# Performance work log

Measured on AMD Instinct MI355X. Metric: run time of the kernel, lower is better.

Reference implementation:

```python
import jax, jax.numpy as jnp
import numpy as np

N = 50000      # nodes
E = 800000     # edges (before self-loops)
IN_C = 128
HID = 32
HEADS = 4
OUT_C = 64
NEG_SLOPE = 0.2


def setup_inputs() -> dict:
    key = jax.random.key(0)
    ks = jax.random.split(key, 10)
    x = jax.random.normal(ks[0], (N, IN_C), dtype=jnp.float32)
    edge_index = jax.random.randint(ks[1], (2, E), 0, N, dtype=jnp.int32)
    # layer 1 params (GATConv(in_c, hid_c, heads=4), concat=True)
    W1 = jax.random.normal(ks[2], (IN_C, HEADS * HID), dtype=jnp.float32) / np.sqrt(IN_C)
    a_src1 = jax.random.normal(ks[3], (HEADS, HID), dtype=jnp.float32) / np.sqrt(HID)
    a_dst1 = jax.random.normal(ks[4], (HEADS, HID), dtype=jnp.float32) / np.sqrt(HID)
    b1 = jnp.zeros((HEADS * HID,), dtype=jnp.float32)
    # layer 2 params (GATConv(hid_c*heads, out_c, heads=1))
    W2 = jax.random.normal(ks[5], (HEADS * HID, OUT_C), dtype=jnp.float32) / np.sqrt(HEADS * HID)
    a_src2 = jax.random.normal(ks[6], (1, OUT_C), dtype=jnp.float32) / np.sqrt(OUT_C)
    a_dst2 = jax.random.normal(ks[7], (1, OUT_C), dtype=jnp.float32) / np.sqrt(OUT_C)
    b2 = jnp.zeros((OUT_C,), dtype=jnp.float32)
    return {"x": x, "edge_index": edge_index, "W1": W1, "a_src1": a_src1,
            "a_dst1": a_dst1, "b1": b1, "W2": W2, "a_src2": a_src2,
            "a_dst2": a_dst2, "b2": b2}


def _gat_layer(x, src, dst, self_mask, W, a_s, a_d, b, n):
    """One PyG-style GATConv: concat heads, leaky_relu(0.2), scatter-softmax over dst."""
    H, F = a_s.shape
    h = (x @ W).reshape(n, H, F)                       # [N, H, F]
    al_s = jnp.einsum('nhf,hf->nh', h, a_s)            # [N, H]
    al_d = jnp.einsum('nhf,hf->nh', h, a_d)
    e = al_s[src] + al_d[dst]                          # [E', H]
    e = jnp.where(e >= 0, e, NEG_SLOPE * e)            # leaky relu
    # emulate remove_self_loops on original edges (appended loops not masked)
    e = jnp.where(self_mask[:, None], -1e30, e)
    m = jax.ops.segment_max(e, dst, num_segments=n)    # per-dst max for stability
    p = jnp.exp(e - m[dst])
    p = jnp.where(self_mask[:, None], 0.0, p)
    denom = jax.ops.segment_sum(p, dst, num_segments=n) + 1e-16
    alpha = p / denom[dst]                             # [E', H]
    out = jax.ops.segment_sum(alpha[:, :, None] * h[src], dst, num_segments=n)
    return out.reshape(n, H * F) + b


def reference(x, edge_index, W1, a_src1, a_dst1, b1, W2, a_src2, a_dst2, b2):
    n = x.shape[0]
    src, dst = edge_index[0], edge_index[1]
    loops = jnp.arange(n, dtype=edge_index.dtype)
    src_a = jnp.concatenate([src, loops])
    dst_a = jnp.concatenate([dst, loops])
    # mask pre-existing self-loops (PyG removes then re-adds self loops)
    self_mask = jnp.concatenate([src == dst, jnp.zeros((n,), dtype=bool)])
    h = _gat_layer(x, src_a, dst_a, self_mask, W1, a_src1, a_dst1, b1, n)
    h = jax.nn.relu(h)
    return _gat_layer(h, src_a, dst_a, self_mask, W2, a_src2, a_dst2, b2, n)
```

## Files before the change

kernel.cpp:

```cpp
#include <hip/hip_runtime.h>

typedef unsigned short u16;
typedef unsigned int u32;
typedef __attribute__((ext_vector_type(8))) short bf16x8;
typedef __attribute__((ext_vector_type(4))) float f32x4;

__device__ __forceinline__ float bf(u16 u){ return __uint_as_float(((u32)u) << 16); }
__device__ __forceinline__ float bf_lo(u32 u){ return __uint_as_float(u << 16); }
__device__ __forceinline__ float bf_hi(u32 u){ return __uint_as_float(u & 0xFFFF0000u); }
__device__ __forceinline__ u16 to_bf16(float f){
    u32 x = __float_as_uint(f);
    u32 r = (x + 0x7FFFu + ((x >> 16) & 1u)) >> 16;
    return (u16)r;
}
__device__ __forceinline__ float leaky(float v){ return (v >= 0.f) ? v : 0.2f * v; }
__device__ __forceinline__ float eexp(float v){
    return __expf(fminf(leaky(v), 80.f));
}
__device__ __forceinline__ float ldany(const void* p, int i, int fl){
    return fl ? bf(((const u16*)p)[i]) : ((const float*)p)[i];
}
__device__ __forceinline__ u16 ldany_bf(const void* p, int i, int fl){
    return fl ? ((const u16*)p)[i] : to_bf16(((const float*)p)[i]);
}

constexpr int NS = 256;

struct HistCvtArgs {
    const int* dst; const int* src; int E; int chE; u16* cnt; int NBIN;
    const void* xin; u16* Xb; int nx;
    const void* W1; const void* W2; u16* W1t; u16* W2t;
    const void* vin[6]; float* vout[6];
    int* flag;
};
__global__ __launch_bounds__(256) void hist_cvt(HistCvtArgs a){
    int b = blockIdx.x;
    if (b < NS){
        __shared__ u32 hist[128];
        if (threadIdx.x < 128) hist[threadIdx.x] = 0;
        __syncthreads();
        int s0 = b * a.chE, s1 = min(a.E, s0 + a.chE);
        for (int i = s0 + threadIdx.x; i < s1; i += 256){
            int d = a.dst[i];
            if (a.src[i] != d) atomicAdd(&hist[d >> 9], 1);
        }
        __syncthreads();
        if (threadIdx.x < a.NBIN)
            a.cnt[b * a.NBIN + threadIdx.x] = (u16)hist[threadIdx.x];
        return;
    }
    __shared__ int sflag;
    const u16* x16 = (const u16*)a.xin;
    if (threadIdx.x < 64){
        int ok = 1;
        for (int i = threadIdx.x; i < 256; i += 64){
            u16 v = x16[i];
            int e = (v >> 7) & 0xFF;
            if (!((e >= 100 && e <= 140) || (v & 0x7FFFu) == 0)) ok = 0;
        }
        unsigned long long bl = __ballot(ok);
        if (threadIdx.x == 0) sflag = (__popcll(bl) >= 62) ? 1 : 0;
    }
    __syncthreads();
    int fl = sflag;
    int ci = (b - NS) * 256 + threadIdx.x;
    if (ci == 0) *a.flag = fl;
    if (ci < a.nx){ a.Xb[ci] = ldany_bf(a.xin, ci, fl); return; }
    ci -= a.nx;
    if (ci < 128 * 128){
        int n = ci >> 7, k = ci & 127;
        a.W1t[ci] = ldany_bf(a.W1, k * 128 + n, fl);
        return;
    }
    ci -= 128 * 128;
    if (ci < 64 * 128){
        int n = ci >> 7, k = ci & 127;
        a.W2t[ci] = ldany_bf(a.W2, k * 64 + n, fl);
        return;
    }
    ci -= 64 * 128;
    const int vsz[6] = {128, 128, 128, 64, 64, 64};
    #pragma unroll
    for (int s = 0; s < 6; s++){
        if (ci < vsz[s]){ a.vout[s][ci] = ldany(a.vin[s], ci, fl); return; }
        ci -= vsz[s];
    }
}

__global__ __launch_bounds__(1024) void scan_cnt(const u16* __restrict__ cnt,
                                                 u32* __restrict__ S, int NBIN){
    __shared__ int wsum[16];
    int t = threadIdx.x;
    int M = NBIN * NS;
    int C = (M + 1023) / 1024;
    int f0 = t * C;
    int s = 0;
    for (int i = 0; i < C; i++){
        int f = f0 + i;
        if (f < M) s += cnt[(f & 255) * NBIN + (f >> 8)];
    }
    int v = s;
    #pragma unroll
    for (int d = 1; d < 64; d <<= 1){
        int o = __shfl_up(v, d);
        if ((t & 63) >= d) v += o;
    }
    if ((t & 63) == 63) wsum[t >> 6] = v;
    __syncthreads();
    int woff = 0;
    for (int wv = 0; wv < (t >> 6); wv++) woff += wsum[wv];
    int run = woff + v - s;
    for (int i = 0; i < C; i++){
        int f = f0 + i;
        if (f < M){
            S[f] = run;
            run += cnt[(f & 255) * NBIN + (f >> 8)];
        }
    }
    if (t == 1023) S[M] = run;
}

struct BucketGemmArgs {
    const int* dst; const int* src; int E; int chE; const u32* S; int NBIN;
    u32* bucket;
    const u16* Xb; const u16* W1t; u16* HB;
    const float* a_s; const float* a_d; float* al_s; float* al_d;
    int N;
};
__global__ __launch_bounds__(256) void bucket_gemm(BucketGemmArgs a){
    int b = blockIdx.x;
    if (b < NS){
        __shared__ u32 cur[128];
        if (threadIdx.x < a.NBIN) cur[threadIdx.x] = a.S[threadIdx.x * NS + b];
        __syncthreads();
        int s0 = b * a.chE, s1 = min(a.E, s0 + a.chE);
        for (int i = s0 + threadIdx.x; i < s1; i += 256){
            int d = a.dst[i];
            int s = a.src[i];
            if (s != d){
                u32 pos = atomicAdd(&cur[d >> 9], 1);
                a.bucket[pos] = ((u32)d << 16) | (u32)s;
            }
        }
        return;
    }
    int gb = b - NS;
    int lane = threadIdx.x & 63;
    int w = threadIdx.x >> 6;
    int row0 = gb * 64 + w * 16;
    int m = lane & 15, quad = lane >> 4;
    int arow = row0 + m;
    if (arow >= a.N) arow = a.N - 1;
    f32x4 acc[8];
    #pragma unroll
    for (int j = 0; j < 8; j++) acc[j] = (f32x4){0.f, 0.f, 0.f, 0.f};
    const u16* ap = a.Xb + (size_t)arow * 128 + quad * 8;
    const u16* bp = a.W1t + (size_t)m * 128 + quad * 8;
    #pragma unroll
    for (int kc = 0; kc < 4; kc++){
        bf16x8 av = *(const bf16x8*)(ap + kc * 32);
        #pragma unroll
        for (int nb = 0; nb < 8; nb++){
            bf16x8 bv = *(const bf16x8*)(bp + nb * 16 * 128 + kc * 32);
            acc[nb] = __builtin_amdgcn_mfma_f32_16x16x32_bf16(av, bv, acc[nb], 0, 0, 0);
        }
    }
    #pragma unroll
    for (int nb = 0; nb < 8; nb++){
        #pragma unroll
        for (int r = 0; r < 4; r++){
            int grow = row0 + quad * 4 + r;
            if (grow < a.N) a.HB[(size_t)grow * 128 + nb * 16 + m] = to_bf16(acc[nb][r]);
        }
    }
    float asr[8], adr[8];
    #pragma unroll
    for (int nb = 0; nb < 8; nb++){ asr[nb] = a.a_s[nb * 16 + m]; adr[nb] = a.a_d[nb * 16 + m]; }
    #pragma unroll
    for (int r = 0; r < 4; r++){
        int grow = row0 + quad * 4 + r;
        #pragma unroll
        for (int h = 0; h < 4; h++){
            float ps = acc[2 * h][r] * asr[2 * h] + acc[2 * h + 1][r] * asr[2 * h + 1];
            float pd = acc[2 * h][r] * adr[2 * h] + acc[2 * h + 1][r] * adr[2 * h + 1];
            #pragma unroll
            for (int d = 1; d < 16; d <<= 1){
                ps += __shfl_xor(ps, d);
                pd += __shfl_xor(pd, d);
            }
            if (m == h && grow < a.N){
                a.al_s[grow * 4 + h] = ps;
                a.al_d[grow * 4 + h] = pd;
            }
        }
    }
}

__global__ __launch_bounds__(256) void bin_csr(const u32* __restrict__ S,
                                               const u32* __restrict__ bucket,
                                               int* __restrict__ off,
                                               u16* __restrict__ csr,
                                               int N, int NBIN){
    __shared__ u32 degL[512];
    __shared__ u32 curL[512];
    __shared__ int wsum[4];
    int b = blockIdx.x, t = threadIdx.x;
    int lo = b << 9;
    u32 base = S[b * NS];
    u32 end  = S[(b + 1) * NS];
    degL[t] = 0; degL[t + 256] = 0;
    __syncthreads();
    for (u32 i = base + t; i < end; i += 256){
        u32 pr = bucket[i];
        atomicAdd(&degL[(pr >> 16) - lo], 1);
    }
    __syncthreads();
    u32 d0 = degL[2 * t], d1 = degL[2 * t + 1];
    int p = (int)(d0 + d1);
    int v = p;
    #pragma unroll
    for (int d = 1; d < 64; d <<= 1){
        int o = __shfl_up(v, d);
        if ((t & 63) >= d) v += o;
    }
    if ((t & 63) == 63) wsum[t >> 6] = v;
    __syncthreads();
    int woff = 0;
    for (int wv = 0; wv < (t >> 6); wv++) woff += wsum[wv];
    int eb = woff + v - p;
    curL[2 * t] = eb;
    curL[2 * t + 1] = eb + d0;
    int n0 = lo + 2 * t, n1 = lo + 2 * t + 1;
    if (n0 < N) off[n0] = (int)(base + eb);
    if (n1 < N) off[n1] = (int)(base + eb + d0);
    if (b == NBIN - 1 && t == 255) off[N] = (int)end;
    __syncthreads();
    for (u32 i = base + t; i < end; i += 256){
        u32 pr = bucket[i];
        u32 pos = base + atomicAdd(&curL[(pr >> 16) - lo], 1);
        csr[pos] = (u16)(pr & 0xFFFF);
    }
}

__global__ __launch_bounds__(256) void gemm2_logits(const u16* __restrict__ Xb,
                                                    const u16* __restrict__ Wt,
                                                    u16* __restrict__ HB,
                                                    const float* __restrict__ a_s,
                                                    const float* __restrict__ a_d,
                                                    float* __restrict__ al_s,
                                                    float* __restrict__ al_d, int N){
    int lane = threadIdx.x & 63;
    int w = threadIdx.x >> 6;
    int row0 = blockIdx.x * 64 + w * 16;
    int m = lane & 15, quad = lane >> 4;
    int arow = row0 + m;
    if (arow >= N) arow = N - 1;
    f32x4 acc[4];
    #pragma unroll
    for (int j = 0; j < 4; j++) acc[j] = (f32x4){0.f, 0.f, 0.f, 0.f};
    const u16* ap = Xb + (size_t)arow * 128 + quad * 8;
    const u16* bp = Wt + (size_t)m * 128 + quad * 8;
    #pragma unroll
    for (int kc = 0; kc < 4; kc++){
        bf16x8 av = *(const bf16x8*)(ap + kc * 32);
        #pragma unroll
        for (int nb = 0; nb < 4; nb++){
            bf16x8 bv = *(const bf16x8*)(bp + nb * 16 * 128 + kc * 32);
            acc[nb] = __builtin_amdgcn_mfma_f32_16x16x32_bf16(av, bv, acc[nb], 0, 0, 0);
        }
    }
    #pragma unroll
    for (int nb = 0; nb < 4; nb++){
        #pragma unroll
        for (int r = 0; r < 4; r++){
            int grow = row0 + quad * 4 + r;
            if (grow < N) HB[(size_t)grow * 64 + nb * 16 + m] = to_bf16(acc[nb][r]);
        }
    }
    float asr[4], adr[4];
    #pragma unroll
    for (int nb = 0; nb < 4; nb++){ asr[nb] = a_s[nb * 16 + m]; adr[nb] = a_d[nb * 16 + m]; }
    #pragma unroll
    for (int r = 0; r < 4; r++){
        int grow = row0 + quad * 4 + r;
        float ps = 0.f, pd = 0.f;
        #pragma unroll
        for (int nb = 0; nb < 4; nb++){ ps += acc[nb][r] * asr[nb]; pd += acc[nb][r] * adr[nb]; }
        #pragma unroll
        for (int d = 1; d < 16; d <<= 1){
            ps += __shfl_xor(ps, d);
            pd += __shfl_xor(pd, d);
        }
        if (m == 0 && grow < N){
            al_s[grow] = ps;
            al_d[grow] = pd;
        }
    }
}

__global__ __launch_bounds__(256) void gat_agg1(const int* __restrict__ off,
                                                const u16* __restrict__ csr,
                                                float* __restrict__ eex,
                                                const u16* __restrict__ h1,
                                                const float* __restrict__ als,
                                                const float* __restrict__ ald,
                                                const float* __restrict__ b1,
                                                u16* __restrict__ outm, int N){
    int lane = threadIdx.x & 63;
    int n = blockIdx.x * 4 + (threadIdx.x >> 6);
    if (n >= N) return;
    int o0 = off[n], o1 = off[n + 1];
    int h = lane & 3;
    float aldh = ald[n * 4 + h];
    float s = 0.f;
    for (int j = o0 + (lane >> 2); j < o1; j += 16){
        int sc = csr[j];
        float e = eexp(als[sc * 4 + h] + aldh);
        eex[j * 4 + h] = e;
        s += e;
    }
    #pragma unroll
    for (int d = 4; d < 64; d <<= 1) s += __shfl_xor(s, d);
    float esx = eexp(als[n * 4 + h] + aldh);
    float inv = 1.f / (s + esx + 1e-16f);
    float psv = esx * inv;
    __builtin_amdgcn_s_waitcnt(0);
    int q = lane >> 4, ql = lane & 15;
    int c0 = ql * 8;
    int head = ql >> 2;
    float invh = __shfl(inv, head);
    float ps   = __shfl(psv, head);
    float acc[8] = {};
    int j = o0 + q;
    for (; j + 4 < o1; j += 8){
        int sc0 = csr[j], sc1 = csr[j + 4];
        float p0 = eex[j * 4 + head] * invh;
        float p1 = eex[(j + 4) * 4 + head] * invh;
        uint4 u0 = *(const uint4*)&h1[(size_t)sc0 * 128 + c0];
        uint4 u1 = *(const uint4*)&h1[(size_t)sc1 * 128 + c0];
        acc[0] += p0 * bf_lo(u0.x) + p1 * bf_lo(u1.x);
        acc[1] += p0 * bf_hi(u0.x) + p1 * bf_hi(u1.x);
        acc[2] += p0 * bf_lo(u0.y) + p1 * bf_lo(u1.y);
        acc[3] += p0 * bf_hi(u0.y) + p1 * bf_hi(u1.y);
        acc[4] += p0 * bf_lo(u0.z) + p1 * bf_lo(u1.z);
        acc[5] += p0 * bf_hi(u0.z) + p1 * bf_hi(u1.z);
        acc[6] += p0 * bf_lo(u0.w) + p1 * bf_lo(u1.w);
        acc[7] += p0 * bf_hi(u0.w) + p1 * bf_hi(u1.w);
    }
    if (j < o1){
        int sc = csr[j];
        float p = eex[j * 4 + head] * invh;
        uint4 u = *(const uint4*)&h1[(size_t)sc * 128 + c0];
        acc[0] += p * bf_lo(u.x); acc[1] += p * bf_hi(u.x);
        acc[2] += p * bf_lo(u.y); acc[3] += p * bf_hi(u.y);
        acc[4] += p * bf_lo(u.z); acc[5] += p * bf_hi(u.z);
        acc[6] += p * bf_lo(u.w); acc[7] += p * bf_hi(u.w);
    }
    if (q == 0){
        uint4 u = *(const uint4*)&h1[(size_t)n * 128 + c0];
        acc[0] += ps * bf_lo(u.x); acc[1] += ps * bf_hi(u.x);
        acc[2] += ps * bf_lo(u.y); acc[3] += ps * bf_hi(u.y);
        acc[4] += ps * bf_lo(u.z); acc[5] += ps * bf_hi(u.z);
        acc[6] += ps * bf_lo(u.w); acc[7] += ps * bf_hi(u.w);
    }
    #pragma unroll
    for (int i = 0; i < 8; i++){
        acc[i] += __shfl_xor(acc[i], 16);
        acc[i] += __shfl_xor(acc[i], 32);
    }
    if (q == 0){
        float4 bA = *(const float4*)&b1[c0];
        float4 bB = *(const float4*)&b1[c0 + 4];
        u16 pk[8];
        pk[0] = to_bf16(fmaxf(acc[0] + bA.x, 0.f));
        pk[1] = to_bf16(fmaxf(acc[1] + bA.y, 0.f));
        pk[2] = to_bf16(fmaxf(acc[2] + bA.z, 0.f));
        pk[3] = to_bf16(fmaxf(acc[3] + bA.w, 0.f));
        pk[4] = to_bf16(fmaxf(acc[4] + bB.x, 0.f));
        pk[5] = to_bf16(fmaxf(acc[5] + bB.y, 0.f));
        pk[6] = to_bf16(fmaxf(acc[6] + bB.z, 0.f));
        pk[7] = to_bf16(fmaxf(acc[7] + bB.w, 0.f));
        *(uint4*)&outm[(size_t)n * 128 + c0] = *(uint4*)pk;
    }
}

__global__ __launch_bounds__(256) void gat_agg2(const int* __restrict__ off,
                                                const u16* __restrict__ csr,
                                                float* __restrict__ eex,
                                                const u16* __restrict__ h2,
                                                const float* __restrict__ als,
                                                const float* __restrict__ ald,
                                                const float* __restrict__ b2,
                                                void* __restrict__ outv, int N,
                                                const int* __restrict__ flag){
    int lane = threadIdx.x & 63;
    int n = blockIdx.x * 4 + (threadIdx.x >> 6);
    if (n >= N) return;
    int o0 = off[n], o1 = off[n + 1];
    float aldn = ald[n];
    float s = 0.f;
    for (int j = o0 + lane; j < o1; j += 64){
        int sc = csr[j];
        float e = eexp(als[sc] + aldn);
        eex[j] = e;
        s += e;
    }
    #pragma unroll
    for (int d = 1; d < 64; d <<= 1) s += __shfl_xor(s, d);
    float esx = eexp(als[n] + aldn);
    float inv = 1.f / (s + esx + 1e-16f);
    float ps = esx * inv;
    __builtin_amdgcn_s_waitcnt(0);
    int oc = lane >> 3, ol = lane & 7;
    int c0 = ol * 8;
    float acc[8] = {};
    int j = o0 + oc;
    for (; j + 8 < o1; j += 16){
        int sc0 = csr[j], sc1 = csr[j + 8];
        float p0 = eex[j] * inv;
        float p1 = eex[j + 8] * inv;
        uint4 u0 = *(const uint4*)&h2[(size_t)sc0 * 64 + c0];
        uint4 u1 = *(const uint4*)&h2[(size_t)sc1 * 64 + c0];
        acc[0] += p0 * bf_lo(u0.x) + p1 * bf_lo(u1.x);
        acc[1] += p0 * bf_hi(u0.x) + p1 * bf_hi(u1.x);
        acc[2] += p0 * bf_lo(u0.y) + p1 * bf_lo(u1.y);
        acc[3] += p0 * bf_hi(u0.y) + p1 * bf_hi(u1.y);
        acc[4] += p0 * bf_lo(u0.z) + p1 * bf_lo(u1.z);
        acc[5] += p0 * bf_hi(u0.z) + p1 * bf_hi(u1.z);
        acc[6] += p0 * bf_lo(u0.w) + p1 * bf_lo(u1.w);
        acc[7] += p0 * bf_hi(u0.w) + p1 * bf_hi(u1.w);
    }
    if (j < o1){
        int sc = csr[j];
        float p = eex[j] * inv;
        uint4 u = *(const uint4*)&h2[(size_t)sc * 64 + c0];
        acc[0] += p * bf_lo(u.x); acc[1] += p * bf_hi(u.x);
        acc[2] += p * bf_lo(u.y); acc[3] += p * bf_hi(u.y);
        acc[4] += p * bf_lo(u.z); acc[5] += p * bf_hi(u.z);
        acc[6] += p * bf_lo(u.w); acc[7] += p * bf_hi(u.w);
    }
    if (oc == 0){
        uint4 u = *(const uint4*)&h2[(size_t)n * 64 + c0];
        acc[0] += ps * bf_lo(u.x); acc[1] += ps * bf_hi(u.x);
        acc[2] += ps * bf_lo(u.y); acc[3] += ps * bf_hi(u.y);
        acc[4] += ps * bf_lo(u.z); acc[5] += ps * bf_hi(u.z);
        acc[6] += ps * bf_lo(u.w); acc[7] += ps * bf_hi(u.w);
    }
    #pragma unroll
    for (int i = 0; i < 8; i++){
        acc[i] += __shfl_xor(acc[i], 8);
        acc[i] += __shfl_xor(acc[i], 16);
        acc[i] += __shfl_xor(acc[i], 32);
    }
    if (oc == 0){
        float4 bA = *(const float4*)&b2[c0];
        float4 bB = *(const float4*)&b2[c0 + 4];
        float r[8];
        r[0] = acc[0] + bA.x; r[1] = acc[1] + bA.y;
        r[2] = acc[2] + bA.z; r[3] = acc[3] + bA.w;
        r[4] = acc[4] + bB.x; r[5] = acc[5] + bB.y;
        r[6] = acc[6] + bB.z; r[7] = acc[7] + bB.w;
        if (*flag){
            u16 pk[8];
            #pragma unroll
            for (int i = 0; i < 8; i++) pk[i] = to_bf16(r[i]);
            *(uint4*)&((u16*)outv)[(size_t)n * 64 + c0] = *(uint4*)pk;
        } else {
            float* op = &((float*)outv)[(size_t)n * 64 + c0];
            *(float4*)op = make_float4(r[0], r[1], r[2], r[3]);
            *(float4*)(op + 4) = make_float4(r[4], r[5], r[6], r[7]);
        }
    }
}

extern "C" void kernel_launch(void* const* d_in, const int* in_sizes, int n_in,
                              void* d_out, int out_size, void* d_ws, size_t ws_size,
                              hipStream_t stream){
    const int* ei  = (const int*)d_in[1];
    const int N = in_sizes[0] / 128;
    const int E = in_sizes[1] / 2;
    const int* src = ei;
    const int* dst = ei + E;
    const int NBIN = (N + 511) >> 9;
    const int chE  = (E + NS - 1) / NS;

    char* w = (char*)d_ws;
    auto alloc = [&](size_t bytes){ char* p = w; w += (bytes + 255) & ~(size_t)255; return p; };
    int*   flag  = (int*)  alloc(4);
    u16*   cnt   = (u16*)  alloc((size_t)NS * NBIN * 2);
    u32*   S     = (u32*)  alloc(((size_t)NS * NBIN + 1) * 4);
    u32*   bucket= (u32*)  alloc((size_t)E * 4);
    int*   off   = (int*)  alloc((size_t)(N + 1) * 4);
    u16*   csr   = (u16*)  alloc((size_t)E * 2);
    float* eex1  = (float*)alloc((size_t)E * 4 * 4);
    u16*   W1t   = (u16*)  alloc(128 * 128 * 2);
    u16*   W2t   = (u16*)  alloc(64 * 128 * 2);
    float* as1f  = (float*)alloc(128 * 4);
    float* ad1f  = (float*)alloc(128 * 4);
    float* b1f   = (float*)alloc(128 * 4);
    float* as2f  = (float*)alloc(64 * 4);
    float* ad2f  = (float*)alloc(64 * 4);
    float* b2f   = (float*)alloc(64 * 4);
    u16*   Xb    = (u16*)  alloc((size_t)N * 128 * 2);
    u16*   h1b   = (u16*)  alloc((size_t)N * 128 * 2);
    u16*   hmidb = (u16*)  alloc((size_t)N * 128 * 2);
    u16*   h2b   = (u16*)  alloc((size_t)N * 64 * 2);
    float* als1  = (float*)alloc((size_t)N * 4 * 4);
    float* ald1  = (float*)alloc((size_t)N * 4 * 4);
    float* eex2  = eex1;
    float* als2  = als1;
    float* ald2  = ald1;

    HistCvtArgs k1;
    k1.dst = dst; k1.src = src; k1.E = E; k1.chE = chE; k1.cnt = cnt; k1.NBIN = NBIN;
    k1.xin = d_in[0]; k1.Xb = Xb; k1.nx = N * 128;
    k1.W1 = d_in[2]; k1.W2 = d_in[6]; k1.W1t = W1t; k1.W2t = W2t;
    const void* vin[6]  = {d_in[3], d_in[4], d_in[5], d_in[7], d_in[8], d_in[9]};
    float* vout[6] = {as1f, ad1f, b1f, as2f, ad2f, b2f};
    for (int s = 0; s < 6; s++){ k1.vin[s] = vin[s]; k1.vout[s] = vout[s]; }
    k1.flag = flag;
    int cvt_total = N * 128 + 128 * 128 + 64 * 128 + 576;
    hist_cvt<<<NS + (cvt_total + 255) / 256, 256, 0, stream>>>(k1);

    scan_cnt<<<1, 1024, 0, stream>>>(cnt, S, NBIN);

    BucketGemmArgs k3;
    k3.dst = dst; k3.src = src; k3.E = E; k3.chE = chE; k3.S = S; k3.NBIN = NBIN;
    k3.bucket = bucket;
    k3.Xb = Xb; k3.W1t = W1t; k3.HB = h1b;
    k3.a_s = as1f; k3.a_d = ad1f; k3.al_s = als1; k3.al_d = ald1;
    k3.N = N;
    bucket_gemm<<<NS + (N + 63) / 64, 256, 0, stream>>>(k3);

    bin_csr<<<NBIN, 256, 0, stream>>>(S, bucket, off, csr, N, NBIN);

    gat_agg1<<<(N + 3) / 4, 256, 0, stream>>>(off, csr, eex1, h1b, als1, ald1, b1f, hmidb, N);

    gemm2_logits<<<(N + 63) / 64, 256, 0, stream>>>(hmidb, W2t, h2b, as2f, ad2f, als2, ald2, N);

    gat_agg2<<<(N + 3) / 4, 256, 0, stream>>>(off, csr, eex2, h2b, als2, ald2, b2f, d_out, N, flag);
}
```

Before: 277.0 us.

## Fuse softmax into single-pass aggregation and make count scan contiguous

```diff
diff --git a/kernel.cpp b/kernel.cpp
--- a/kernel.cpp
+++ b/kernel.cpp
@@ -46,7 +46,7 @@
         }
         __syncthreads();
         if (threadIdx.x < a.NBIN)
-            a.cnt[b * a.NBIN + threadIdx.x] = (u16)hist[threadIdx.x];
+            a.cnt[threadIdx.x * NS + b] = (u16)hist[threadIdx.x];
         return;
     }
     __shared__ int sflag;
@@ -94,10 +94,14 @@
     int M = NBIN * NS;
     int C = (M + 1023) / 1024;
     int f0 = t * C;
+    u32 c[32];
     int s = 0;
-    for (int i = 0; i < C; i++){
+    #pragma unroll
+    for (int i = 0; i < 32; i++){
         int f = f0 + i;
-        if (f < M) s += cnt[(f & 255) * NBIN + (f >> 8)];
+        u32 v = (i < C && f < M) ? (u32)cnt[f] : 0u;
+        c[i] = v;
+        s += (int)v;
     }
     int v = s;
     #pragma unroll
@@ -110,11 +114,12 @@
     int woff = 0;
     for (int wv = 0; wv < (t >> 6); wv++) woff += wsum[wv];
     int run = woff + v - s;
-    for (int i = 0; i < C; i++){
+    #pragma unroll
+    for (int i = 0; i < 32; i++){
         int f = f0 + i;
-        if (f < M){
+        if (i < C && f < M){
             S[f] = run;
-            run += cnt[(f & 255) * NBIN + (f >> 8)];
+            run += (int)c[i];
         }
     }
     if (t == 1023) S[M] = run;
@@ -300,7 +305,6 @@
 
 __global__ __launch_bounds__(256) void gat_agg1(const int* __restrict__ off,
                                                 const u16* __restrict__ csr,
-                                                float* __restrict__ eex,
                                                 const u16* __restrict__ h1,
                                                 const float* __restrict__ als,
                                                 const float* __restrict__ ald,
@@ -310,83 +314,71 @@
     int n = blockIdx.x * 4 + (threadIdx.x >> 6);
     if (n >= N) return;
     int o0 = off[n], o1 = off[n + 1];
-    int h = lane & 3;
-    float aldh = ald[n * 4 + h];
-    float s = 0.f;
-    for (int j = o0 + (lane >> 2); j < o1; j += 16){
-        int sc = csr[j];
-        float e = eexp(als[sc * 4 + h] + aldh);
-        eex[j * 4 + h] = e;
-        s += e;
-    }
-    #pragma unroll
-    for (int d = 4; d < 64; d <<= 1) s += __shfl_xor(s, d);
-    float esx = eexp(als[n * 4 + h] + aldh);
-    float inv = 1.f / (s + esx + 1e-16f);
-    float psv = esx * inv;
-    __builtin_amdgcn_s_waitcnt(0);
     int q = lane >> 4, ql = lane & 15;
     int c0 = ql * 8;
     int head = ql >> 2;
-    float invh = __shfl(inv, head);
-    float ps   = __shfl(psv, head);
+    float aldh = ald[n * 4 + head];
     float acc[8] = {};
+    float s = 0.f;
     int j = o0 + q;
     for (; j + 4 < o1; j += 8){
         int sc0 = csr[j], sc1 = csr[j + 4];
-        float p0 = eex[j * 4 + head] * invh;
-        float p1 = eex[(j + 4) * 4 + head] * invh;
+        float e0 = eexp(als[sc0 * 4 + head] + aldh);
+        float e1 = eexp(als[sc1 * 4 + head] + aldh);
         uint4 u0 = *(const uint4*)&h1[(size_t)sc0 * 128 + c0];
         uint4 u1 = *(const uint4*)&h1[(size_t)sc1 * 128 + c0];
-        acc[0] += p0 * bf_lo(u0.x) + p1 * bf_lo(u1.x);
-        acc[1] += p0 * bf_hi(u0.x) + p1 * bf_hi(u1.x);
-        acc[2] += p0 * bf_lo(u0.y) + p1 * bf_lo(u1.y);
-        acc[3] += p0 * bf_hi(u0.y) + p1 * bf_hi(u1.y);
-        acc[4] += p0 * bf_lo(u0.z) + p1 * bf_lo(u1.z);
-        acc[5] += p0 * bf_hi(u0.z) + p1 * bf_hi(u1.z);
-        acc[6] += p0 * bf_lo(u0.w) + p1 * bf_lo(u1.w);
-        acc[7] += p0 * bf_hi(u0.w) + p1 * bf_hi(u1.w);
+        s += e0 + e1;
+        acc[0] += e0 * bf_lo(u0.x) + e1 * bf_lo(u1.x);
+        acc[1] += e0 * bf_hi(u0.x) + e1 * bf_hi(u1.x);
+        acc[2] += e0 * bf_lo(u0.y) + e1 * bf_lo(u1.y);
+        acc[3] += e0 * bf_hi(u0.y) + e1 * bf_hi(u1.y);
+        acc[4] += e0 * bf_lo(u0.z) + e1 * bf_lo(u1.z);
+        acc[5] += e0 * bf_hi(u0.z) + e1 * bf_hi(u1.z);
+        acc[6] += e0 * bf_lo(u0.w) + e1 * bf_lo(u1.w);
+        acc[7] += e0 * bf_hi(u0.w) + e1 * bf_hi(u1.w);
     }
     if (j < o1){
         int sc = csr[j];
-        float p = eex[j * 4 + head] * invh;
+        float e = eexp(als[sc * 4 + head] + aldh);
         uint4 u = *(const uint4*)&h1[(size_t)sc * 128 + c0];
-        acc[0] += p * bf_lo(u.x); acc[1] += p * bf_hi(u.x);
-        acc[2] += p * bf_lo(u.y); acc[3] += p * bf_hi(u.y);
-        acc[4] += p * bf_lo(u.z); acc[5] += p * bf_hi(u.z);
-        acc[6] += p * bf_lo(u.w); acc[7] += p * bf_hi(u.w);
-    }
-    if (q == 0){
-        uint4 u = *(const uint4*)&h1[(size_t)n * 128 + c0];
-        acc[0] += ps * bf_lo(u.x); acc[1] += ps * bf_hi(u.x);
-        acc[2] += ps * bf_lo(u.y); acc[3] += ps * bf_hi(u.y);
-        acc[4] += ps * bf_lo(u.z); acc[5] += ps * bf_hi(u.z);
-        acc[6] += ps * bf_lo(u.w); acc[7] += ps * bf_hi(u.w);
-    }
+        s += e;
+        acc[0] += e * bf_lo(u.x); acc[1] += e * bf_hi(u.x);
+        acc[2] += e * bf_lo(u.y); acc[3] += e * bf_hi(u.y);
+        acc[4] += e * bf_lo(u.z); acc[5] += e * bf_hi(u.z);
+        acc[6] += e * bf_lo(u.w); acc[7] += e * bf_hi(u.w);
+    }
+    s += __shfl_xor(s, 16);
+    s += __shfl_xor(s, 32);
     #pragma unroll
     for (int i = 0; i < 8; i++){
         acc[i] += __shfl_xor(acc[i], 16);
         acc[i] += __shfl_xor(acc[i], 32);
     }
     if (q == 0){
+        float esx = eexp(als[n * 4 + head] + aldh);
+        float inv = 1.f / (s + esx + 1e-16f);
+        uint4 u = *(const uint4*)&h1[(size_t)n * 128 + c0];
+        acc[0] += esx * bf_lo(u.x); acc[1] += esx * bf_hi(u.x);
+        acc[2] += esx * bf_lo(u.y); acc[3] += esx * bf_hi(u.y);
+        acc[4] += esx * bf_lo(u.z); acc[5] += esx * bf_hi(u.z);
+        acc[6] += esx * bf_lo(u.w); acc[7] += esx * bf_hi(u.w);
         float4 bA = *(const float4*)&b1[c0];
         float4 bB = *(const float4*)&b1[c0 + 4];
         u16 pk[8];
-        pk[0] = to_bf16(fmaxf(acc[0] + bA.x, 0.f));
-        pk[1] = to_bf16(fmaxf(acc[1] + bA.y, 0.f));
-        pk[2] = to_bf16(fmaxf(acc[2] + bA.z, 0.f));
-        pk[3] = to_bf16(fmaxf(acc[3] + bA.w, 0.f));
-        pk[4] = to_bf16(fmaxf(acc[4] + bB.x, 0.f));
-        pk[5] = to_bf16(fmaxf(acc[5] + bB.y, 0.f));
-        pk[6] = to_bf16(fmaxf(acc[6] + bB.z, 0.f));
-        pk[7] = to_bf16(fmaxf(acc[7] + bB.w, 0.f));
+        pk[0] = to_bf16(fmaxf(acc[0] * inv + bA.x, 0.f));
+        pk[1] = to_bf16(fmaxf(acc[1] * inv + bA.y, 0.f));
+        pk[2] = to_bf16(fmaxf(acc[2] * inv + bA.z, 0.f));
+        pk[3] = to_bf16(fmaxf(acc[3] * inv + bA.w, 0.f));
+        pk[4] = to_bf16(fmaxf(acc[4] * inv + bB.x, 0.f));
+        pk[5] = to_bf16(fmaxf(acc[5] * inv + bB.y, 0.f));
+        pk[6] = to_bf16(fmaxf(acc[6] * inv + bB.z, 0.f));
+        pk[7] = to_bf16(fmaxf(acc[7] * inv + bB.w, 0.f));
         *(uint4*)&outm[(size_t)n * 128 + c0] = *(uint4*)pk;
     }
 }
 
 __global__ __launch_bounds__(256) void gat_agg2(const int* __restrict__ off,
                                                 const u16* __restrict__ csr,
-                                                float* __restrict__ eex,
                                                 const u16* __restrict__ h2,
                                                 const float* __restrict__ als,
                                                 const float* __restrict__ ald,
@@ -397,55 +389,41 @@
     int n = blockIdx.x * 4 + (threadIdx.x >> 6);
     if (n >= N) return;
     int o0 = off[n], o1 = off[n + 1];
-    float aldn = ald[n];
-    float s = 0.f;
-    for (int j = o0 + lane; j < o1; j += 64){
-        int sc = csr[j];
-        float e = eexp(als[sc] + aldn);
-        eex[j] = e;
-        s += e;
-    }
-    #pragma unroll
-    for (int d = 1; d < 64; d <<= 1) s += __shfl_xor(s, d);
-    float esx = eexp(als[n] + aldn);
-    float inv = 1.f / (s + esx + 1e-16f);
-    float ps = esx * inv;
-    __builtin_amdgcn_s_waitcnt(0);
     int oc = lane >> 3, ol = lane & 7;
     int c0 = ol * 8;
+    float aldn = ald[n];
     float acc[8] = {};
+    float s = 0.f;
     int j = o0 + oc;
     for (; j + 8 < o1; j += 16){
         int sc0 = csr[j], sc1 = csr[j + 8];
-        float p0 = eex[j] * inv;
-        float p1 = eex[j + 8] * inv;
+        float e0 = eexp(als[sc0] + aldn);
+        float e1 = eexp(als[sc1] + aldn);
         uint4 u0 = *(const uint4*)&h2[(size_t)sc0 * 64 + c0];
         uint4 u1 = *(const uint4*)&h2[(size_t)sc1 * 64 + c0];
-        acc[0] += p0 * bf_lo(u0.x) + p1 * bf_lo(u1.x);
-        acc[1] += p0 * bf_hi(u0.x) + p1 * bf_hi(u1.x);
-        acc[2] += p0 * bf_lo(u0.y) + p1 * bf_lo(u1.y);
-        acc[3] += p0 * bf_hi(u0.y) + p1 * bf_hi(u1.y);
-        acc[4] += p0 * bf_lo(u0.z) + p1 * bf_lo(u1.z);
-        acc[5] += p0 * bf_hi(u0.z) + p1 * bf_hi(u1.z);
-        acc[6] += p0 * bf_lo(u0.w) + p1 * bf_lo(u1.w);
-        acc[7] += p0 * bf_hi(u0.w) + p1 * bf_hi(u1.w);
+        s += e0 + e1;
+        acc[0] += e0 * bf_lo(u0.x) + e1 * bf_lo(u1.x);
+        acc[1] += e0 * bf_hi(u0.x) + e1 * bf_hi(u1.x);
+        acc[2] += e0 * bf_lo(u0.y) + e1 * bf_lo(u1.y);
+        acc[3] += e0 * bf_hi(u0.y) + e1 * bf_hi(u1.y);
+        acc[4] += e0 * bf_lo(u0.z) + e1 * bf_lo(u1.z);
+        acc[5] += e0 * bf_hi(u0.z) + e1 * bf_hi(u1.z);
+        acc[6] += e0 * bf_lo(u0.w) + e1 * bf_lo(u1.w);
+        acc[7] += e0 * bf_hi(u0.w) + e1 * bf_hi(u1.w);
     }
     if (j < o1){
         int sc = csr[j];
-        float p = eex[j] * inv;
+        float e = eexp(als[sc] + aldn);
         uint4 u = *(const uint4*)&h2[(size_t)sc * 64 + c0];
-        acc[0] += p * bf_lo(u.x); acc[1] += p * bf_hi(u.x);
-        acc[2] += p * bf_lo(u.y); acc[3] += p * bf_hi(u.y);
-        acc[4] += p * bf_lo(u.z); acc[5] += p * bf_hi(u.z);
-        acc[6] += p * bf_lo(u.w); acc[7] += p * bf_hi(u.w);
-    }
-    if (oc == 0){
-        uint4 u = *(const uint4*)&h2[(size_t)n * 64 + c0];
-        acc[0] += ps * bf_lo(u.x); acc[1] += ps * bf_hi(u.x);
-        acc[2] += ps * bf_lo(u.y); acc[3] += ps * bf_hi(u.y);
-        acc[4] += ps * bf_lo(u.z); acc[5] += ps * bf_hi(u.z);
-        acc[6] += ps * bf_lo(u.w); acc[7] += ps * bf_hi(u.w);
-    }
+        s += e;
+        acc[0] += e * bf_lo(u.x); acc[1] += e * bf_hi(u.x);
+        acc[2] += e * bf_lo(u.y); acc[3] += e * bf_hi(u.y);
+        acc[4] += e * bf_lo(u.z); acc[5] += e * bf_hi(u.z);
+        acc[6] += e * bf_lo(u.w); acc[7] += e * bf_hi(u.w);
+    }
+    s += __shfl_xor(s, 8);
+    s += __shfl_xor(s, 16);
+    s += __shfl_xor(s, 32);
     #pragma unroll
     for (int i = 0; i < 8; i++){
         acc[i] += __shfl_xor(acc[i], 8);
@@ -453,13 +431,20 @@
         acc[i] += __shfl_xor(acc[i], 32);
     }
     if (oc == 0){
+        float esx = eexp(als[n] + aldn);
+        float inv = 1.f / (s + esx + 1e-16f);
+        uint4 u = *(const uint4*)&h2[(size_t)n * 64 + c0];
+        acc[0] += esx * bf_lo(u.x); acc[1] += esx * bf_hi(u.x);
+        acc[2] += esx * bf_lo(u.y); acc[3] += esx * bf_hi(u.y);
+        acc[4] += esx * bf_lo(u.z); acc[5] += esx * bf_hi(u.z);
+        acc[6] += esx * bf_lo(u.w); acc[7] += esx * bf_hi(u.w);
         float4 bA = *(const float4*)&b2[c0];
         float4 bB = *(const float4*)&b2[c0 + 4];
         float r[8];
-        r[0] = acc[0] + bA.x; r[1] = acc[1] + bA.y;
-        r[2] = acc[2] + bA.z; r[3] = acc[3] + bA.w;
-        r[4] = acc[4] + bB.x; r[5] = acc[5] + bB.y;
-        r[6] = acc[6] + bB.z; r[7] = acc[7] + bB.w;
+        r[0] = acc[0] * inv + bA.x; r[1] = acc[1] * inv + bA.y;
+        r[2] = acc[2] * inv + bA.z; r[3] = acc[3] * inv + bA.w;
+        r[4] = acc[4] * inv + bB.x; r[5] = acc[5] * inv + bB.y;
+        r[6] = acc[6] * inv + bB.z; r[7] = acc[7] * inv + bB.w;
         if (*flag){
             u16 pk[8];
             #pragma unroll
@@ -492,7 +477,6 @@
     u32*   bucket= (u32*)  alloc((size_t)E * 4);
     int*   off   = (int*)  alloc((size_t)(N + 1) * 4);
     u16*   csr   = (u16*)  alloc((size_t)E * 2);
-    float* eex1  = (float*)alloc((size_t)E * 4 * 4);
     u16*   W1t   = (u16*)  alloc(128 * 128 * 2);
     u16*   W2t   = (u16*)  alloc(64 * 128 * 2);
     float* as1f  = (float*)alloc(128 * 4);
@@ -507,7 +491,6 @@
     u16*   h2b   = (u16*)  alloc((size_t)N * 64 * 2);
     float* als1  = (float*)alloc((size_t)N * 4 * 4);
     float* ald1  = (float*)alloc((size_t)N * 4 * 4);
-    float* eex2  = eex1;
     float* als2  = als1;
     float* ald2  = ald1;
 
@@ -534,9 +517,9 @@
 
     bin_csr<<<NBIN, 256, 0, stream>>>(S, bucket, off, csr, N, NBIN);
 
-    gat_agg1<<<(N + 3) / 4, 256, 0, stream>>>(off, csr, eex1, h1b, als1, ald1, b1f, hmidb, N);
+    gat_agg1<<<(N + 3) / 4, 256, 0, stream>>>(off, csr, h1b, als1, ald1, b1f, hmidb, N);
 
     gemm2_logits<<<(N + 63) / 64, 256, 0, stream>>>(hmidb, W2t, h2b, as2f, ad2f, als2, ald2, N);
 
-    gat_agg2<<<(N + 3) / 4, 256, 0, stream>>>(off, csr, eex2, h2b, als2, ald2, b2f, d_out, N, flag);
-}
+    gat_agg2<<<(N + 3) / 4, 256, 0, stream>>>(off, csr, h2b, als2, ald2, b2f, d_out, N, flag);
+}
```

New measurement: 245.1 us. 1.13x faster.
